# Kernel optimization log

Hardware: AMD Instinct MI355X
Metric: run time of the kernel (lower is better)

The kernel has to match this reference:

```python
import jax, jax.numpy as jnp
import numpy as np

BN_EPS = 1e-5

def batch_norm(x, gamma, beta):
    # training-mode BatchNorm1d: biased batch stats over the edge dim
    mean = jnp.mean(x, axis=0)
    var = jnp.var(x, axis=0)
    return (x - mean) * jax.lax.rsqrt(var + BN_EPS) * gamma + beta

def setup_inputs() -> dict:
    key = jax.random.key(0)
    ks = jax.random.split(key, 10)
    N, F, E = 50000, 128, 600000
    D_in = 2 * F + 12  # 268
    h = jax.random.normal(ks[0], (N, F), dtype=jnp.float32)
    edge_feature = jax.random.normal(ks[1], (E, 12), dtype=jnp.float32)
    src = jax.random.randint(ks[2], (E,), 0, N)
    dst = jax.random.randint(ks[3], (E,), 0, N)
    def lin(k, fan_in, shape):
        bound = 1.0 / np.sqrt(fan_in)
        return jax.random.uniform(k, shape, jnp.float32, -bound, bound)
    W1 = lin(ks[4], D_in, (28, D_in)); b1 = lin(ks[5], D_in, (28,))
    W2 = lin(ks[6], 28, (8, 28));      b2 = lin(ks[7], 28, (8,))
    W3 = lin(ks[8], 8, (1, 8));        b3 = lin(ks[9], 8, (1,))
    gamma1 = jnp.ones((28,), jnp.float32); beta1 = jnp.zeros((28,), jnp.float32)
    gamma2 = jnp.ones((8,), jnp.float32);  beta2 = jnp.zeros((8,), jnp.float32)
    return {"h": h, "edge_feature": edge_feature, "src": src, "dst": dst,
            "W1": W1, "b1": b1, "gamma1": gamma1, "beta1": beta1,
            "W2": W2, "b2": b2, "gamma2": gamma2, "beta2": beta2,
            "W3": W3, "b3": b3}

def reference(h, edge_feature, src, dst, W1, b1, gamma1, beta1,
              W2, b2, gamma2, beta2, W3, b3):
    h_u = h[src]                    # [E, F] gather of source node feats
    h_v = h[dst]                    # [E, F] gather of dest node feats
    x = jnp.concatenate([h_u, h_v, edge_feature], axis=1)  # [E, 2F+12]
    s = jax.nn.relu(batch_norm(x @ W1.T + b1, gamma1, beta1))  # [E, 28]
    s = jax.nn.relu(batch_norm(s @ W2.T + b2, gamma2, beta2))  # [E, 8]
    score = s @ W3.T + b3           # [E, 1]
    return score
```

## Files before the change

### kernel.cpp

```cpp
#include <hip/hip_runtime.h>

#define BN_EPS 1e-5f


__global__ void k1_proj(const float* __restrict__ h, const float* __restrict__ W1,
                        float* __restrict__ Psrc, float* __restrict__ Pdst,
                        float* __restrict__ stats, int N) {
  __shared__ float lwk[3584];
  if (blockIdx.x == 0 && threadIdx.x < 72) stats[threadIdx.x] = 0.f;
  const int half = blockIdx.x & 1;
  for (int j = threadIdx.x * 4; j < 3584; j += 1024) {
    const int c = j >> 7, k = j & 127;
    *(float4*)&lwk[j] = *(const float4*)(W1 + c * 268 + half * 128 + k);
  }
  __syncthreads();
  const int node = (blockIdx.x >> 1) * 256 + threadIdx.x;
  if (node >= N) return;

  const float4* __restrict__ h4 = (const float4*)(h + (size_t)node * 128);
  float acc[28];
#pragma unroll
  for (int c = 0; c < 28; c++) acc[c] = 0.f;

  for (int kk = 0; kk < 16; kk++) {
    const float4 a = h4[kk * 2];
    const float4 b = h4[kk * 2 + 1];
#pragma unroll
    for (int c = 0; c < 28; c++) {
      const float4 w0 = *(const float4*)&lwk[c * 128 + kk * 8];
      const float4 w1 = *(const float4*)&lwk[c * 128 + kk * 8 + 4];
      acc[c] += a.x * w0.x + a.y * w0.y + a.z * w0.z + a.w * w0.w
              + b.x * w1.x + b.y * w1.y + b.z * w1.z + b.w * w1.w;
    }
  }

  float4* po = (float4*)((half ? Pdst : Psrc) + (size_t)node * 32);
#pragma unroll
  for (int q = 0; q < 7; q++) {
    po[q] = make_float4(acc[q * 4], acc[q * 4 + 1], acc[q * 4 + 2], acc[q * 4 + 3]);
  }
  po[7] = make_float4(0.f, 0.f, 0.f, 0.f);
}

__global__ __launch_bounds__(256)
void k2_edge(const float* __restrict__ Psrc, const float* __restrict__ Pdst,
             const float* __restrict__ ef,
             const int* __restrict__ src, const int* __restrict__ dst,
             const float* __restrict__ W1, const float* __restrict__ b1,
             float* __restrict__ y1, float* __restrict__ stats, int E) {
  __shared__ float lw[28][12];
  __shared__ float lb[28];
  __shared__ float tile[7168];
  __shared__ float lsum[8][28], lssq[8][28];
  const int tid = threadIdx.x;
  for (int i = tid; i < 336; i += 256) lw[i / 12][i % 12] = W1[(i / 12) * 268 + 256 + (i % 12)];
  if (tid < 28) lb[tid] = b1[tid];
  if (tid < 224) { lsum[tid / 28][tid % 28] = 0.f; lssq[tid / 28][tid % 28] = 0.f; }
  __syncthreads();

  float sx = 0.f, sy = 0.f, sz = 0.f, sw = 0.f;
  float qx = 0.f, qy = 0.f, qz = 0.f, qw = 0.f;

  const int base = blockIdx.x * 256;
  const int e = base + tid;
  if (e < E) {
    const int s = src[e], d = dst[e];
    const float4* __restrict__ pa4 = (const float4*)(Psrc + (size_t)s * 32);
    const float4* __restrict__ pb4 = (const float4*)(Pdst + (size_t)d * 32);
    const float4* __restrict__ e4 = (const float4*)(ef + (size_t)e * 12);
    float f[12];
#pragma unroll
    for (int q = 0; q < 3; q++) {
      const float4 v = e4[q];
      f[q * 4] = v.x; f[q * 4 + 1] = v.y; f[q * 4 + 2] = v.z; f[q * 4 + 3] = v.w;
    }
    float* tr = &tile[tid * 28];
#pragma unroll
    for (int q = 0; q < 7; q++) {
      const float4 ta = pa4[q];
      const float4 tb = pb4[q];
      float vv[4];
#pragma unroll
      for (int i2 = 0; i2 < 4; i2++) {
        const int c = q * 4 + i2;
        const float4* lw4 = (const float4*)(&lw[c][0]);
        const float4 w0 = lw4[0], w1 = lw4[1], w2 = lw4[2];
        vv[i2] = lb[c]
            + f[0] * w0.x + f[1] * w0.y + f[2] * w0.z + f[3] * w0.w
            + f[4] * w1.x + f[5] * w1.y + f[6] * w1.z + f[7] * w1.w
            + f[8] * w2.x + f[9] * w2.y + f[10] * w2.z + f[11] * w2.w;
      }
      *(float4*)&tr[q * 4] = make_float4(vv[0] + ta.x + tb.x, vv[1] + ta.y + tb.y,
                                         vv[2] + ta.z + tb.z, vv[3] + ta.w + tb.w);
    }
  }
  __syncthreads();
  const int nval = min(256, E - base) * 28;
  if (tid < 224) {
    const size_t gbase = (size_t)base * 28;
#pragma unroll
    for (int i = 0; i < 8; i++) {
      const int jl = tid * 4 + i * 896;
      if (jl < nval) {
        const float4 v = *(const float4*)&tile[jl];
        *(float4*)(y1 + gbase + jl) = v;
        sx += v.x; sy += v.y; sz += v.z; sw += v.w;
        qx += v.x * v.x; qy += v.y * v.y; qz += v.z * v.z; qw += v.w * v.w;
      }
    }
  }

  if (tid < 224) {
    const int c0 = (tid * 4) % 28, a8 = tid / 28;
    atomicAdd(&lsum[a8][c0], sx);     atomicAdd(&lssq[a8][c0], qx);
    atomicAdd(&lsum[a8][c0 + 1], sy); atomicAdd(&lssq[a8][c0 + 1], qy);
    atomicAdd(&lsum[a8][c0 + 2], sz); atomicAdd(&lssq[a8][c0 + 2], qz);
    atomicAdd(&lsum[a8][c0 + 3], sw); atomicAdd(&lssq[a8][c0 + 3], qw);
  }
  __syncthreads();
  if (tid < 28) {
    float S = 0.f, Q = 0.f;
#pragma unroll
    for (int a = 0; a < 8; a++) { S += lsum[a][tid]; Q += lssq[a][tid]; }
    atomicAdd(&stats[tid], S);
    atomicAdd(&stats[28 + tid], Q);
  }
}

__global__ void k4_l2(const float* __restrict__ y1, const float* __restrict__ statsRO,
                      const float* __restrict__ W2, const float* __restrict__ b2,
                      const float* __restrict__ g1, const float* __restrict__ be1,
                      float* __restrict__ y2, float* __restrict__ statsW,
                      int E, float invE) {
  __shared__ float tile[7168];
  __shared__ float4 w2q[8][7];
  __shared__ float scs[28], shs[28];
  __shared__ float lb2[8];
  const int tid = threadIdx.x;
  if (tid < 56) {
    w2q[tid / 7][tid % 7] = *(const float4*)(W2 + (tid / 7) * 28 + (tid % 7) * 4);
  } else if (tid >= 64 && tid < 92) {
    const int c = tid - 64;
    const float mean = statsRO[c] * invE;
    const float var = statsRO[28 + c] * invE - mean * mean;
    const float sc = g1[c] * rsqrtf(var + BN_EPS);
    scs[c] = sc;
    shs[c] = be1[c] - mean * sc;
  } else if (tid >= 96 && tid < 104) {
    lb2[tid - 96] = b2[tid - 96];
  }
  float as[8], aq[8];
#pragma unroll
  for (int o = 0; o < 8; o++) { as[o] = 0.f; aq[o] = 0.f; }

  for (int t = 0; t < 2; t++) {
    const int base = (blockIdx.x * 2 + t) * 256;
    const int nval = min(256, E - base) * 28;
    __syncthreads();
    if (tid < 224) {
      const size_t gbase = (size_t)base * 28;
#pragma unroll
      for (int i = 0; i < 8; i++) {
        const int jl = tid * 4 + i * 896;
        if (jl < nval) *(float4*)&tile[jl] = *(const float4*)(y1 + gbase + jl);
      }
    }
    __syncthreads();
    const int e = base + tid;
    if (e < E) {
      float accv[8];
#pragma unroll
      for (int o = 0; o < 8; o++) accv[o] = lb2[o];
      const float* tr = &tile[tid * 28];
#pragma unroll
      for (int q = 0; q < 7; q++) {
        const float4 sv = *(const float4*)&tr[q * 4];
        const float4 sc = *(const float4*)&scs[q * 4];
        const float4 sh = *(const float4*)&shs[q * 4];
        const float s0 = fmaxf(sv.x * sc.x + sh.x, 0.f);
        const float s1 = fmaxf(sv.y * sc.y + sh.y, 0.f);
        const float s2 = fmaxf(sv.z * sc.z + sh.z, 0.f);
        const float s3 = fmaxf(sv.w * sc.w + sh.w, 0.f);
#pragma unroll
        for (int o = 0; o < 8; o++) {
          const float4 w = w2q[o][q];
          accv[o] += s0 * w.x + s1 * w.y + s2 * w.z + s3 * w.w;
        }
      }
      float4* yo = (float4*)(y2 + (size_t)e * 8);
      yo[0] = make_float4(accv[0], accv[1], accv[2], accv[3]);
      yo[1] = make_float4(accv[4], accv[5], accv[6], accv[7]);
#pragma unroll
      for (int o = 0; o < 8; o++) { as[o] += accv[o]; aq[o] += accv[o] * accv[o]; }
    }
  }

#pragma unroll
  for (int o = 0; o < 8; o++) {
    for (int off = 32; off; off >>= 1) {
      as[o] += __shfl_down(as[o], off);
      aq[o] += __shfl_down(aq[o], off);
    }
  }
  __shared__ float redS[4][16];
  const int wave = tid >> 6, lane = tid & 63;
  if (lane == 0) {
#pragma unroll
    for (int o = 0; o < 8; o++) { redS[wave][o] = as[o]; redS[wave][8 + o] = aq[o]; }
  }
  __syncthreads();
  if (tid < 16) {
    atomicAdd(&statsW[56 + tid], redS[0][tid] + redS[1][tid] + redS[2][tid] + redS[3][tid]);
  }
}

__global__ void k6_l3(const float* __restrict__ y2, const float* __restrict__ stats,
                      const float* __restrict__ g2, const float* __restrict__ be2,
                      const float* __restrict__ W3, const float* __restrict__ b3,
                      float* __restrict__ out, int E, float invE) {
  __shared__ float sc2[8], sh2[8], w3[8];
  __shared__ float b3s;
  if (threadIdx.x < 8) {
    const int c = threadIdx.x;
    const float mean = stats[56 + c] * invE;
    const float var = stats[64 + c] * invE - mean * mean;
    const float sc = g2[c] * rsqrtf(var + BN_EPS);
    sc2[c] = sc;
    sh2[c] = be2[c] - mean * sc;
    w3[c] = W3[c];
    if (c == 0) b3s = b3[0];
  }
  __syncthreads();
  const int e = blockIdx.x * blockDim.x + threadIdx.x;
  if (e >= E) return;
  const float4* p = (const float4*)(y2 + (size_t)e * 8);
  float4 a = p[0], b4 = p[1];
  float v[8] = {a.x, a.y, a.z, a.w, b4.x, b4.y, b4.z, b4.w};
  float acc = b3s;
#pragma unroll
  for (int o = 0; o < 8; o++) {
    float s = fmaxf(v[o] * sc2[o] + sh2[o], 0.f);
    acc += w3[o] * s;
  }
  out[e] = acc;
}

extern "C" void kernel_launch(void* const* d_in, const int* in_sizes, int n_in,
                              void* d_out, int out_size, void* d_ws, size_t ws_size,
                              hipStream_t stream) {
  const float* h   = (const float*)d_in[0];
  const float* ef  = (const float*)d_in[1];
  const int* src   = (const int*)d_in[2];
  const int* dst   = (const int*)d_in[3];
  const float* W1  = (const float*)d_in[4];
  const float* b1  = (const float*)d_in[5];
  const float* g1  = (const float*)d_in[6];
  const float* be1 = (const float*)d_in[7];
  const float* W2  = (const float*)d_in[8];
  const float* b2  = (const float*)d_in[9];
  const float* g2  = (const float*)d_in[10];
  const float* be2 = (const float*)d_in[11];
  const float* W3  = (const float*)d_in[12];
  const float* b3  = (const float*)d_in[13];
  float* out = (float*)d_out;

  const int N = in_sizes[0] / 128;
  const int E = in_sizes[2];
  const float invE = 1.0f / (float)E;

  float* ws = (float*)d_ws;
  float* stats = ws;
  float* Psrc = ws + 256;
  float* y1 = Psrc + (size_t)N * 32;
  float* y2 = y1 + (size_t)E * 28;
  float* Pdst = y2;

  const int nodeBlocks = (N + 255) / 256;
  const int nTiles = (E + 255) / 256;
  const int nPair = (nTiles + 1) / 2;
  k1_proj<<<nodeBlocks * 2, 256, 0, stream>>>(h, W1, Psrc, Pdst, stats, N);
  k2_edge<<<nTiles, 256, 0, stream>>>(Psrc, Pdst, ef, src, dst, W1, b1, y1, stats, E);
  k4_l2<<<nPair, 256, 0, stream>>>(y1, stats, W2, b2, g1, be1, y2, stats, E, invE);
  k6_l3<<<nTiles, 256, 0, stream>>>(y2, stats, g2, be2, W3, b3, out, E, invE);
}
```

Before: 282.9 us.

## Process two edge tiles per block in k2 and use an 8-lane shuffle mapping in k4

Result: slower. 293.5 us (+3.7%).

```diff
diff --git a/kernel.cpp b/kernel.cpp
--- a/kernel.cpp
+++ b/kernel.cpp
@@ -61,53 +61,56 @@
   float sx = 0.f, sy = 0.f, sz = 0.f, sw = 0.f;
   float qx = 0.f, qy = 0.f, qz = 0.f, qw = 0.f;
 
-  const int base = blockIdx.x * 256;
-  const int e = base + tid;
-  if (e < E) {
-    const int s = src[e], d = dst[e];
-    const float4* __restrict__ pa4 = (const float4*)(Psrc + (size_t)s * 32);
-    const float4* __restrict__ pb4 = (const float4*)(Pdst + (size_t)d * 32);
-    const float4* __restrict__ e4 = (const float4*)(ef + (size_t)e * 12);
-    float f[12];
-#pragma unroll
-    for (int q = 0; q < 3; q++) {
-      const float4 v = e4[q];
-      f[q * 4] = v.x; f[q * 4 + 1] = v.y; f[q * 4 + 2] = v.z; f[q * 4 + 3] = v.w;
-    }
-    float* tr = &tile[tid * 28];
-#pragma unroll
-    for (int q = 0; q < 7; q++) {
-      const float4 ta = pa4[q];
-      const float4 tb = pb4[q];
-      float vv[4];
-#pragma unroll
-      for (int i2 = 0; i2 < 4; i2++) {
-        const int c = q * 4 + i2;
-        const float4* lw4 = (const float4*)(&lw[c][0]);
-        const float4 w0 = lw4[0], w1 = lw4[1], w2 = lw4[2];
-        vv[i2] = lb[c]
-            + f[0] * w0.x + f[1] * w0.y + f[2] * w0.z + f[3] * w0.w
-            + f[4] * w1.x + f[5] * w1.y + f[6] * w1.z + f[7] * w1.w
-            + f[8] * w2.x + f[9] * w2.y + f[10] * w2.z + f[11] * w2.w;
+  for (int t = 0; t < 2; t++) {
+    const int base = (blockIdx.x * 2 + t) * 256;
+    const int e = base + tid;
+    if (e < E) {
+      const int s = src[e], d = dst[e];
+      const float4* __restrict__ pa4 = (const float4*)(Psrc + (size_t)s * 32);
+      const float4* __restrict__ pb4 = (const float4*)(Pdst + (size_t)d * 32);
+      const float4* __restrict__ e4 = (const float4*)(ef + (size_t)e * 12);
+      float f[12];
+#pragma unroll
+      for (int q = 0; q < 3; q++) {
+        const float4 v = e4[q];
+        f[q * 4] = v.x; f[q * 4 + 1] = v.y; f[q * 4 + 2] = v.z; f[q * 4 + 3] = v.w;
       }
-      *(float4*)&tr[q * 4] = make_float4(vv[0] + ta.x + tb.x, vv[1] + ta.y + tb.y,
-                                         vv[2] + ta.z + tb.z, vv[3] + ta.w + tb.w);
-    }
-  }
-  __syncthreads();
-  const int nval = min(256, E - base) * 28;
-  if (tid < 224) {
-    const size_t gbase = (size_t)base * 28;
-#pragma unroll
-    for (int i = 0; i < 8; i++) {
-      const int jl = tid * 4 + i * 896;
-      if (jl < nval) {
-        const float4 v = *(const float4*)&tile[jl];
-        *(float4*)(y1 + gbase + jl) = v;
-        sx += v.x; sy += v.y; sz += v.z; sw += v.w;
-        qx += v.x * v.x; qy += v.y * v.y; qz += v.z * v.z; qw += v.w * v.w;
+      float* tr = &tile[tid * 28];
+#pragma unroll
+      for (int q = 0; q < 7; q++) {
+        const float4 ta = pa4[q];
+        const float4 tb = pb4[q];
+        float vv[4];
+#pragma unroll
+        for (int i2 = 0; i2 < 4; i2++) {
+          const int c = q * 4 + i2;
+          const float4* lw4 = (const float4*)(&lw[c][0]);
+          const float4 w0 = lw4[0], w1 = lw4[1], w2 = lw4[2];
+          vv[i2] = lb[c]
+              + f[0] * w0.x + f[1] * w0.y + f[2] * w0.z + f[3] * w0.w
+              + f[4] * w1.x + f[5] * w1.y + f[6] * w1.z + f[7] * w1.w
+              + f[8] * w2.x + f[9] * w2.y + f[10] * w2.z + f[11] * w2.w;
+        }
+        *(float4*)&tr[q * 4] = make_float4(vv[0] + ta.x + tb.x, vv[1] + ta.y + tb.y,
+                                           vv[2] + ta.z + tb.z, vv[3] + ta.w + tb.w);
       }
     }
+    __syncthreads();
+    const int nval = min(256, E - base) * 28;
+    if (tid < 224) {
+      const size_t gbase = (size_t)base * 28;
+#pragma unroll
+      for (int i = 0; i < 8; i++) {
+        const int jl = tid * 4 + i * 896;
+        if (jl < nval) {
+          const float4 v = *(const float4*)&tile[jl];
+          *(float4*)(y1 + gbase + jl) = v;
+          sx += v.x; sy += v.y; sz += v.z; sw += v.w;
+          qx += v.x * v.x; qy += v.y * v.y; qz += v.z * v.z; qw += v.w * v.w;
+        }
+      }
+    }
+    __syncthreads();
   }
 
   if (tid < 224) {
@@ -127,12 +130,12 @@
   }
 }
 
-__global__ void k4_l2(const float* __restrict__ y1, const float* __restrict__ statsRO,
-                      const float* __restrict__ W2, const float* __restrict__ b2,
-                      const float* __restrict__ g1, const float* __restrict__ be1,
-                      float* __restrict__ y2, float* __restrict__ statsW,
-                      int E, float invE) {
-  __shared__ float tile[7168];
+__global__ __launch_bounds__(256)
+void k4_l2(const float* __restrict__ y1, const float* __restrict__ statsRO,
+           const float* __restrict__ W2, const float* __restrict__ b2,
+           const float* __restrict__ g1, const float* __restrict__ be1,
+           float* __restrict__ y2, float* __restrict__ statsW,
+           int E, float invE) {
   __shared__ float4 w2q[8][7];
   __shared__ float scs[28], shs[28];
   __shared__ float lb2[8];
@@ -149,49 +152,61 @@
   } else if (tid >= 96 && tid < 104) {
     lb2[tid - 96] = b2[tid - 96];
   }
+  __syncthreads();
+
+  const int lane = tid & 63;
+  const int q = lane & 7;
+  const bool act = (q < 7);
+  const int eg = lane >> 3;
+  const int waveId = (blockIdx.x * 256 + tid) >> 6;
+  const int nWaves = gridDim.x * 4;
+
+  float4 sc4 = make_float4(0.f, 0.f, 0.f, 0.f);
+  float4 sh4 = make_float4(0.f, 0.f, 0.f, 0.f);
+  float4 wv[8];
+#pragma unroll
+  for (int o = 0; o < 8; o++) wv[o] = make_float4(0.f, 0.f, 0.f, 0.f);
+  if (act) {
+    sc4 = *(const float4*)&scs[q * 4];
+    sh4 = *(const float4*)&shs[q * 4];
+#pragma unroll
+    for (int o = 0; o < 8; o++) wv[o] = w2q[o][q];
+  }
+  float bb[8];
+#pragma unroll
+  for (int o = 0; o < 8; o++) bb[o] = lb2[o];
+
   float as[8], aq[8];
 #pragma unroll
   for (int o = 0; o < 8; o++) { as[o] = 0.f; aq[o] = 0.f; }
 
-  for (int t = 0; t < 2; t++) {
-    const int base = (blockIdx.x * 2 + t) * 256;
-    const int nval = min(256, E - base) * 28;
-    __syncthreads();
-    if (tid < 224) {
-      const size_t gbase = (size_t)base * 28;
-#pragma unroll
-      for (int i = 0; i < 8; i++) {
-        const int jl = tid * 4 + i * 896;
-        if (jl < nval) *(float4*)&tile[jl] = *(const float4*)(y1 + gbase + jl);
-      }
-    }
-    __syncthreads();
-    const int e = base + tid;
-    if (e < E) {
-      float accv[8];
-#pragma unroll
-      for (int o = 0; o < 8; o++) accv[o] = lb2[o];
-      const float* tr = &tile[tid * 28];
-#pragma unroll
-      for (int q = 0; q < 7; q++) {
-        const float4 sv = *(const float4*)&tr[q * 4];
-        const float4 sc = *(const float4*)&scs[q * 4];
-        const float4 sh = *(const float4*)&shs[q * 4];
-        const float s0 = fmaxf(sv.x * sc.x + sh.x, 0.f);
-        const float s1 = fmaxf(sv.y * sc.y + sh.y, 0.f);
-        const float s2 = fmaxf(sv.z * sc.z + sh.z, 0.f);
-        const float s3 = fmaxf(sv.w * sc.w + sh.w, 0.f);
-#pragma unroll
-        for (int o = 0; o < 8; o++) {
-          const float4 w = w2q[o][q];
-          accv[o] += s0 * w.x + s1 * w.y + s2 * w.z + s3 * w.w;
-        }
-      }
+  for (int base = waveId * 8; base < E; base += nWaves * 8) {
+    const int e = base + eg;
+    float4 v = make_float4(0.f, 0.f, 0.f, 0.f);
+    if (act && e < E) v = *(const float4*)(y1 + (size_t)e * 28 + q * 4);
+    const float s0 = fmaxf(v.x * sc4.x + sh4.x, 0.f);
+    const float s1 = fmaxf(v.y * sc4.y + sh4.y, 0.f);
+    const float s2 = fmaxf(v.z * sc4.z + sh4.z, 0.f);
+    const float s3 = fmaxf(v.w * sc4.w + sh4.w, 0.f);
+    float r[8];
+#pragma unroll
+    for (int o = 0; o < 8; o++) {
+      float p = s0 * wv[o].x + s1 * wv[o].y + s2 * wv[o].z + s3 * wv[o].w;
+      p += __shfl_down(p, 4);
+      p += __shfl_down(p, 2);
+      p += __shfl_down(p, 1);
+      r[o] = p;
+    }
+    if (q == 0 && e < E) {
+      const float o0 = r[0] + bb[0], o1 = r[1] + bb[1], o2 = r[2] + bb[2], o3 = r[3] + bb[3];
+      const float o4 = r[4] + bb[4], o5 = r[5] + bb[5], o6 = r[6] + bb[6], o7 = r[7] + bb[7];
       float4* yo = (float4*)(y2 + (size_t)e * 8);
-      yo[0] = make_float4(accv[0], accv[1], accv[2], accv[3]);
-      yo[1] = make_float4(accv[4], accv[5], accv[6], accv[7]);
-#pragma unroll
-      for (int o = 0; o < 8; o++) { as[o] += accv[o]; aq[o] += accv[o] * accv[o]; }
+      yo[0] = make_float4(o0, o1, o2, o3);
+      yo[1] = make_float4(o4, o5, o6, o7);
+      as[0] += o0; aq[0] += o0 * o0; as[1] += o1; aq[1] += o1 * o1;
+      as[2] += o2; aq[2] += o2 * o2; as[3] += o3; aq[3] += o3 * o3;
+      as[4] += o4; aq[4] += o4 * o4; as[5] += o5; aq[5] += o5 * o5;
+      as[6] += o6; aq[6] += o6 * o6; as[7] += o7; aq[7] += o7 * o7;
     }
   }
 
@@ -203,7 +218,7 @@
     }
   }
   __shared__ float redS[4][16];
-  const int wave = tid >> 6, lane = tid & 63;
+  const int wave = tid >> 6;
   if (lane == 0) {
 #pragma unroll
     for (int o = 0; o < 8; o++) { redS[wave][o] = as[o]; redS[wave][8 + o] = aq[o]; }
@@ -279,7 +294,7 @@
   const int nTiles = (E + 255) / 256;
   const int nPair = (nTiles + 1) / 2;
   k1_proj<<<nodeBlocks * 2, 256, 0, stream>>>(h, W1, Psrc, Pdst, stats, N);
-  k2_edge<<<nTiles, 256, 0, stream>>>(Psrc, Pdst, ef, src, dst, W1, b1, y1, stats, E);
-  k4_l2<<<nPair, 256, 0, stream>>>(y1, stats, W2, b2, g1, be1, y2, stats, E, invE);
+  k2_edge<<<nPair, 256, 0, stream>>>(Psrc, Pdst, ef, src, dst, W1, b1, y1, stats, E);
+  k4_l2<<<nTiles, 256, 0, stream>>>(y1, stats, W2, b2, g1, be1, y2, stats, E, invE);
   k6_l3<<<nTiles, 256, 0, stream>>>(y2, stats, g2, be2, W3, b3, out, E, invE);
 }
```
